# Kernel optimization log

Measured on AMD Instinct MI355X. Metric: run time of the kernel, lower is better.

Reference implementation:

```python
import jax, jax.numpy as jnp
import numpy as np

WS = 8          # window size
HEADS = 12      # attention heads
DIM = 768
HEAD_DIM = DIM // HEADS
EPS = 1e-5      # torch nn.LayerNorm default


def _layernorm(x, w, b):
    m = x.mean(-1, keepdims=True)
    v = ((x - m) ** 2).mean(-1, keepdims=True)
    return (x - m) / jnp.sqrt(v + EPS) * w + b


def setup_inputs() -> dict:
    key = jax.random.key(0)
    ks = jax.random.split(key, 8)
    s = 0.02  # weight init scale for numerical sanity
    dim, hd, ws = DIM, HEAD_DIM, WS
    return {
        "x": jax.random.normal(ks[0], (2, 16, 16, 16, dim), jnp.float32),
        "w_qkv": jax.random.normal(ks[1], (dim, 3 * dim), jnp.float32) * s,
        "b_qkv": jnp.zeros((3 * dim,), jnp.float32),
        "w_proj": jax.random.normal(ks[2], (dim, dim), jnp.float32) * s,
        "b_proj": jnp.zeros((dim,), jnp.float32),
        "rel_pos_d": jax.random.normal(ks[3], (2 * ws - 1, hd), jnp.float32) * s,
        "rel_pos_h": jax.random.normal(ks[4], (2 * ws - 1, hd), jnp.float32) * s,
        "rel_pos_w": jax.random.normal(ks[5], (2 * ws - 1, hd), jnp.float32) * s,
        "norm1_w": jnp.ones((dim,), jnp.float32),
        "norm1_b": jnp.zeros((dim,), jnp.float32),
        "norm2_w": jnp.ones((dim,), jnp.float32),
        "norm2_b": jnp.zeros((dim,), jnp.float32),
        "w1": jax.random.normal(ks[6], (dim, 4 * dim), jnp.float32) * s,
        "b1": jnp.zeros((4 * dim,), jnp.float32),
        "w2": jax.random.normal(ks[7], (4 * dim, dim), jnp.float32) * s,
        "b2": jnp.zeros((dim,), jnp.float32),
    }


def reference(x, w_qkv, b_qkv, w_proj, b_proj, rel_pos_d, rel_pos_h, rel_pos_w,
              norm1_w, norm1_b, norm2_w, norm2_b, w1, b1, w2, b2):
    B, D, H, W, C = x.shape
    ws, h = WS, HEADS
    hd = C // h
    scale = hd ** -0.5
    N = ws ** 3

    shortcut = x
    xn = _layernorm(x, norm1_w, norm1_b)

    # window partition (dims divide evenly -> no padding)
    xw = xn.reshape(B, D // ws, ws, H // ws, ws, W // ws, ws, C)
    xw = xw.transpose(0, 1, 3, 5, 2, 4, 6, 7).reshape(-1, N, C)  # [Bw, N, C]
    Bw = xw.shape[0]

    qkv = (xw @ w_qkv + b_qkv).reshape(Bw, N, 3, h, hd)
    qkv = qkv.transpose(2, 0, 3, 1, 4).reshape(3, Bw * h, N, hd)
    q, k, v = qkv[0], qkv[1], qkv[2]  # each [Bw*h, N, hd]

    attn = jnp.einsum('bqc,bkc->bqk', q * scale, k)  # [Bw*h, N, N]

    # decomposed relative position bias; q_size == k_size == ws, so no interp
    idx = jnp.arange(ws)[:, None] - jnp.arange(ws)[None, :] + (ws - 1)  # [ws, ws]
    Rd, Rh, Rw = rel_pos_d[idx], rel_pos_h[idx], rel_pos_w[idx]  # [ws, ws, hd]
    rq = q.reshape(Bw * h, ws, ws, ws, hd)
    rel_d = jnp.einsum('bdhwc,dkc->bdhwk', rq, Rd)
    rel_h = jnp.einsum('bdhwc,hkc->bdhwk', rq, Rh)
    rel_w = jnp.einsum('bdhwc,wkc->bdhwk', rq, Rw)
    attn = (attn.reshape(Bw * h, ws, ws, ws, ws, ws, ws)
            + rel_d[:, :, :, :, :, None, None]
            + rel_h[:, :, :, :, None, :, None]
            + rel_w[:, :, :, :, None, None, :]).reshape(Bw * h, N, N)

    attn = jax.nn.softmax(attn, axis=-1)
    out = (attn @ v).reshape(Bw, h, ws, ws, ws, hd)
    out = out.transpose(0, 2, 3, 4, 1, 5).reshape(Bw, N, C)
    out = out @ w_proj + b_proj

    # window unpartition
    out = out.reshape(B, D // ws, H // ws, W // ws, ws, ws, ws, C)
    out = out.transpose(0, 1, 4, 2, 5, 3, 6, 7).reshape(B, D, H, W, C)

    x = shortcut + out
    xn2 = _layernorm(x, norm2_w, norm2_b)
    # torch nn.GELU default is exact erf GELU
    x = x + (jax.nn.gelu(xn2 @ w1 + b1, approximate=False) @ w2 + b2)
    return x
```

## Files before the change

### kernel.cpp

```cpp
#include <hip/hip_runtime.h>
#include <hip/hip_bf16.h>
#include <math.h>

typedef short s16x8 __attribute__((ext_vector_type(8)));
typedef float f32x4 __attribute__((ext_vector_type(4)));
typedef int   s32x4 __attribute__((ext_vector_type(4)));

#define DIM 768
#define HEADS 12

static __device__ __forceinline__ short f2bf(float x) {
    union { float f; unsigned u; } v; v.f = x;
    unsigned r = (v.u + 0x7FFF + ((v.u >> 16) & 1)) >> 16;
    return (short)r;
}
static __device__ __forceinline__ float bf2f(short x) {
    union { unsigned u; float f; } v;
    v.u = ((unsigned)(unsigned short)x) << 16;
    return v.f;
}
static __device__ __forceinline__ unsigned cvt_pk_bf16(float lo, float hi) {
    unsigned r;
    asm("v_cvt_pk_bf16_f32 %0, %1, %2" : "=v"(r) : "v"(lo), "v"(hi));
    return r;
}

#define GLDS16(g, l) __builtin_amdgcn_global_load_lds( \
    (__attribute__((address_space(1))) void*)(g), \
    (__attribute__((address_space(3))) void*)(l), 16, 0, 0)

static __device__ __forceinline__ int nat_row(int t) {
    int w = t >> 9, n = t & 511;
    int b = w >> 3, dO = (w >> 2) & 1, hO = (w >> 1) & 1, wO = w & 1;
    int di = n >> 6, hi = (n >> 3) & 7, wi = n & 7;
    int Dd = dO * 8 + di, Hh = hO * 8 + hi, Ww = wO * 8 + wi;
    return ((b * 16 + Dd) * 16 + Hh) * 16 + Ww;
}

__global__ __launch_bounds__(256) void transpose_cvt(
    const float* __restrict__ in, short* __restrict__ out, int K, int N) {
    __shared__ float tile[32][33];
    int n0 = blockIdx.x * 32, k0 = blockIdx.y * 32;
    int tx = threadIdx.x & 31, ty = threadIdx.x >> 5;
#pragma unroll
    for (int j = 0; j < 4; j++) {
        int r = ty + j * 8;
        tile[r][tx] = in[(size_t)(k0 + r) * N + n0 + tx];
    }
    __syncthreads();
#pragma unroll
    for (int j = 0; j < 4; j++) {
        int r = ty + j * 8;
        out[(size_t)(n0 + r) * K + k0 + tx] = f2bf(tile[tx][r]);
    }
}

template<int PART>
__global__ __launch_bounds__(256) void ln_kernel(
    const float* __restrict__ x, const float* __restrict__ gw,
    const float* __restrict__ gb, short* __restrict__ out) {
    int t = blockIdx.x;
    int row = PART ? nat_row(t) : t;
    const float* xr = x + (size_t)row * DIM;
    float v0 = xr[threadIdx.x], v1 = xr[threadIdx.x + 256], v2 = xr[threadIdx.x + 512];
    float s1 = v0 + v1 + v2;
    float s2 = v0 * v0 + v1 * v1 + v2 * v2;
#pragma unroll
    for (int o = 32; o > 0; o >>= 1) { s1 += __shfl_down(s1, o); s2 += __shfl_down(s2, o); }
    __shared__ float ws1[4], ws2[4];
    int wid = threadIdx.x >> 6, lane = threadIdx.x & 63;
    if (lane == 0) { ws1[wid] = s1; ws2[wid] = s2; }
    __syncthreads();
    s1 = ws1[0] + ws1[1] + ws1[2] + ws1[3];
    s2 = ws2[0] + ws2[1] + ws2[2] + ws2[3];
    float mean = s1 * (1.f / DIM);
    float var = s2 * (1.f / DIM) - mean * mean;
    float inv = rsqrtf(var + 1e-5f);
    short* orow = out + (size_t)t * DIM;
    orow[threadIdx.x]       = f2bf((v0 - mean) * inv * gw[threadIdx.x]       + gb[threadIdx.x]);
    orow[threadIdx.x + 256] = f2bf((v1 - mean) * inv * gw[threadIdx.x + 256] + gb[threadIdx.x + 256]);
    orow[threadIdx.x + 512] = f2bf((v2 - mean) * inv * gw[threadIdx.x + 512] + gb[threadIdx.x + 512]);
}

enum { EPI_C = 0, EPI_PROJ = 1, EPI_GELU = 2, EPI_MLP2 = 3 };

template<int EPI, int K, int N, int BN>
__global__ __launch_bounds__(256) void gemm_kernel(
    const short* __restrict__ A, const short* __restrict__ BT,
    const float* __restrict__ bias,
    const float* __restrict__ x_in, float* __restrict__ out_f,
    short* __restrict__ out_b) {
    constexpr int GX = N / BN;
    constexpr int NW = BN / 32;
    constexpr int NT = K / 64;
    __shared__ short As[2][128 * 64];
    __shared__ short Bs[2][BN * 64];
    int flat = blockIdx.x;
    int cpx = gridDim.x >> 3;
    int swz = (flat & 7) * cpx + (flat >> 3);
    int tile_n = swz % GX, tile_m = swz / GX;
    int tid = threadIdx.x;
    int wid = tid >> 6, lane = tid & 63, lr = lane & 15, lg = lane >> 4;
    int wr = wid >> 1, wc = wid & 1;
    f32x4 acc[4][NW] = {};
    const short* Arow = A + (size_t)(tile_m * 128) * K;
    const short* Brow = BT + (size_t)(tile_n * BN) * K;
    int swzS = ((lane & 7) ^ ((tid >> 3) & 7)) * 8;
    const short* gA[4]; int ldsOA[4];
#pragma unroll
    for (int i = 0; i < 4; i++) {
        int row = (i * 256 + tid) >> 3;
        gA[i] = Arow + (size_t)row * K + swzS;
        ldsOA[i] = (i * 256 + wid * 64) * 8;
    }
    const short* gB[NW]; int ldsOB[NW];
#pragma unroll
    for (int i = 0; i < NW; i++) {
        int row = (i * 256 + tid) >> 3;
        gB[i] = Brow + (size_t)row * K + swzS;
        ldsOB[i] = (i * 256 + wid * 64) * 8;
    }
    auto stage = [&](int buf, int k0) {
#pragma unroll
        for (int i = 0; i < 4; i++) GLDS16(gA[i] + k0, &As[buf][ldsOA[i]]);
#pragma unroll
        for (int i = 0; i < NW; i++) GLDS16(gB[i] + k0, &Bs[buf][ldsOB[i]]);
    };
    stage(0, 0);
    __syncthreads();
#pragma unroll 1
    for (int t = 0; t < NT; t++) {
        int cur = t & 1;
        if (t + 1 < NT) stage(cur ^ 1, (t + 1) * 64);
#pragma unroll
        for (int h = 0; h < 2; h++) {
            s16x8 af[4], bfr[NW];
#pragma unroll
            for (int m = 0; m < 4; m++) {
                int row = wr * 64 + m * 16 + lr;
                af[m] = *(const s16x8*)&As[cur][row * 64 + (((h * 4 + lg) ^ (lr & 7)) << 3)];
            }
#pragma unroll
            for (int n = 0; n < NW; n++) {
                int row = wc * (BN / 2) + n * 16 + lr;
                bfr[n] = *(const s16x8*)&Bs[cur][row * 64 + (((h * 4 + lg) ^ (lr & 7)) << 3)];
            }
#pragma unroll
            for (int m = 0; m < 4; m++)
#pragma unroll
                for (int n = 0; n < NW; n++)
                    acc[m][n] = __builtin_amdgcn_mfma_f32_16x16x32_bf16(af[m], bfr[n], acc[m][n], 0, 0, 0);
        }
        __syncthreads();
    }
#pragma unroll
    for (int m = 0; m < 4; m++)
#pragma unroll
        for (int n = 0; n < NW; n++)
#pragma unroll
            for (int r = 0; r < 4; r++) {
                int row = tile_m * 128 + wr * 64 + m * 16 + lg * 4 + r;
                int col = tile_n * BN + wc * (BN / 2) + n * 16 + lr;
                float v = acc[m][n][r] + bias[col];
                if (EPI == EPI_C) {
                    out_b[(size_t)row * N + col] = f2bf(v);
                } else if (EPI == EPI_PROJ) {
                    int nr = nat_row(row);
                    out_f[(size_t)nr * DIM + col] = v + x_in[(size_t)nr * DIM + col];
                } else if (EPI == EPI_GELU) {
                    float u = v * (0.7978845608f + 0.0356774081f * v * v);
                    float e = __expf(2.f * u);
                    float g = v - v * __builtin_amdgcn_rcpf(1.f + e);
                    out_b[(size_t)row * (size_t)N + col] = f2bf(g);
                } else {
                    out_f[(size_t)row * DIM + col] += v;
                }
            }
}

__global__ __launch_bounds__(256) void repack_vt(
    const short* __restrict__ qkv, short* __restrict__ vt) {
    __shared__ short tile[64][72];
    int ntb = blockIdx.x, wh = blockIdx.y;
    int win = wh / HEADS, h = wh % HEADS;
    const short* vbase = qkv + (size_t)(win * 512 + ntb * 64) * 2304 + 1536 + h * 64;
    int tid = threadIdx.x;
#pragma unroll
    for (int p = 0; p < 2; p++) {
        int idx = tid + p * 256;
        int tok = idx >> 3, vc = idx & 7;
        s16x8 v = *(const s16x8*)&vbase[(size_t)tok * 2304 + vc * 8];
#pragma unroll
        for (int j = 0; j < 8; j++) tile[vc * 8 + j][tok] = v[j];
    }
    __syncthreads();
#pragma unroll
    for (int p = 0; p < 2; p++) {
        int idx = tid + p * 256;
        int d = idx >> 3, vc = idx & 7;
        s16x8 o = *(const s16x8*)&tile[d][vc * 8];
        *(s16x8*)&vt[((size_t)wh * 64 + d) * 512 + ntb * 64 + vc * 8] = o;
    }
}

__global__ __launch_bounds__(256) void attn_kernel(
    const short* __restrict__ qkv, const short* __restrict__ vt,
    const float* __restrict__ rpd, const float* __restrict__ rph,
    const float* __restrict__ rpw, short* __restrict__ out) {
    __shared__ float bdT[8][128], bhT[8][128], bwT[8][128];
    __shared__ short Rs[48 * 64];
    __shared__ short Ks[2][64 * 64];
    __shared__ short Vs[2][64 * 64];
    int qt2 = blockIdx.x;
    int wh = blockIdx.y;
    int win = wh / HEADS, h = wh % HEADS;
    int qbase = qt2 * 128;
    const short* qp = qkv + (size_t)(win * 512) * 2304 + h * 64;
    const short* kp = qp + 768;
    const short* vp = vt + (size_t)wh * 64 * 512;
    int tid = threadIdx.x, wid = tid >> 6, lane = tid & 63, lr = lane & 15, lg = lane >> 4;
    const float LOG2E = 1.4426950408889634f;

    s16x8 aq[2][2];
#pragma unroll
    for (int g = 0; g < 2; g++) {
        size_t qoff = (size_t)(qbase + g * 64 + wid * 16 + lr) * 2304;
        aq[g][0] = *(const s16x8*)&qp[qoff + lg * 8];
        aq[g][1] = *(const s16x8*)&qp[qoff + 32 + lg * 8];
    }

    for (int i = tid; i < 48 * 64; i += 256) {
        int row = i >> 6, c = i & 63;
        float v = 0.f;
        if (row < 9)                     v = rpd[(qt2 * 2 + row) * 64 + c];
        else if (row >= 16 && row < 31)  v = rph[(row - 16) * 64 + c];
        else if (row >= 32 && row < 47)  v = rpw[(row - 32) * 64 + c];
        Rs[row * 64 + ((((c >> 3) ^ (row & 7)) << 3) | (c & 7))] = f2bf(v * LOG2E);
    }
    __syncthreads();

    int row0 = wid * 8 + (lane >> 3);
    int swz = ((lane & 7) ^ (row0 & 7)) * 8;
    const short* kSrc0 = kp + (size_t)row0 * 2304 + swz;
    const short* kSrc1 = kp + (size_t)(row0 + 32) * 2304 + swz;
    const short* vSrc0 = vp + (size_t)row0 * 512 + swz;
    const short* vSrc1 = vp + (size_t)(row0 + 32) * 512 + swz;
    int ldsOff0 = wid * 512, ldsOff1 = 2048 + wid * 512;

    GLDS16(kSrc0, &Ks[0][ldsOff0]);
    GLDS16(kSrc1, &Ks[0][ldsOff1]);
    GLDS16(vSrc0, &Vs[0][ldsOff0]);
    GLDS16(vSrc1, &Vs[0][ldsOff1]);

    {
        f32x4 G[3][2];
#pragma unroll
        for (int t = 0; t < 3; t++) {
            int arow = t * 16 + lr;
            s16x8 a0 = *(const s16x8*)&Rs[arow * 64 + ((lg ^ (arow & 7)) << 3)];
            s16x8 a1 = *(const s16x8*)&Rs[arow * 64 + (((4 + lg) ^ (arow & 7)) << 3)];
#pragma unroll
            for (int g = 0; g < 2; g++) {
                f32x4 z = {};
                z = __builtin_amdgcn_mfma_f32_16x16x32_bf16(a0, aq[g][0], z, 0, 0, 0);
                z = __builtin_amdgcn_mfma_f32_16x16x32_bf16(a1, aq[g][1], z, 0, 0, 0);
                G[t][g] = z;
            }
        }
        int qcH = (wid * 2 + (lr >> 3)) & 7;
        int qcW = lr & 7;
#pragma unroll
        for (int g = 0; g < 2; g++) {
            int qr = g * 64 + wid * 16 + lr;
#pragma unroll
            for (int r = 0; r < 4; r++) {
                int j = lg * 4 + r;
                int kd = g + 7 - j;
                if (kd >= 0 && kd < 8) bdT[kd][qr] = G[0][g][r];
                int kh = qcH + 7 - j;
                if (kh >= 0 && kh < 8) bhT[kh][qr] = G[1][g][r];
                int kw = qcW + 7 - j;
                if (kw >= 0 && kw < 8) bwT[kw][qr] = G[2][g][r];
            }
        }
    }
    __syncthreads();

    float m_run[2] = {-1e30f, -1e30f}, l_run[2] = {0.f, 0.f};
    f32x4 accO[2][4] = {};
    int sel = lg >> 1;
    const float SC = 0.125f * LOG2E;

#pragma unroll 1
    for (int kt = 0; kt < 8; kt++) {
        int cur = kt & 1;
        if (kt < 7) {
            size_t kAdv = (size_t)(kt + 1) * 64 * 2304;
            int vAdv = (kt + 1) * 64;
            GLDS16(kSrc0 + kAdv, &Ks[cur ^ 1][ldsOff0]);
            GLDS16(kSrc1 + kAdv, &Ks[cur ^ 1][ldsOff1]);
            GLDS16(vSrc0 + vAdv, &Vs[cur ^ 1][ldsOff0]);
            GLDS16(vSrc1 + vAdv, &Vs[cur ^ 1][ldsOff1]);
        }
        f32x4 sa[2][4];
#pragma unroll
        for (int kn = 0; kn < 4; kn++) {
            int krow = kn * 16 + lr;
            const short* kb_ = &Ks[cur][krow * 64];
            s16x8 ak0 = *(const s16x8*)&kb_[((lg ^ (krow & 7)) << 3)];
            s16x8 ak1 = *(const s16x8*)&kb_[(((4 + lg) ^ (krow & 7)) << 3)];
#pragma unroll
            for (int g = 0; g < 2; g++) {
                f32x4 z = {};
                z = __builtin_amdgcn_mfma_f32_16x16x32_bf16(ak0, aq[g][0], z, 0, 0, 0);
                z = __builtin_amdgcn_mfma_f32_16x16x32_bf16(ak1, aq[g][1], z, 0, 0, 0);
                sa[g][kn] = z;
            }
        }
        s32x4 pb[2][2];
#pragma unroll
        for (int g = 0; g < 2; g++) {
            int qr = g * 64 + wid * 16 + lr;
            float bdv = bdT[kt][qr];
            float bb[4], bwv[4];
#pragma unroll
            for (int kn = 0; kn < 4; kn++) bb[kn] = bdv + bhT[2 * kn + sel][qr];
#pragma unroll
            for (int r = 0; r < 4; r++) bwv[r] = bwT[4 * (lg & 1) + r][qr];
            float sv[4][4], mx = -1e30f;
#pragma unroll
            for (int kn = 0; kn < 4; kn++)
#pragma unroll
                for (int r = 0; r < 4; r++) {
                    float vv = sa[g][kn][r] * SC + (bb[kn] + bwv[r]);
                    sv[kn][r] = vv;
                    mx = fmaxf(mx, vv);
                }
            mx = fmaxf(mx, __shfl_xor(mx, 16));
            mx = fmaxf(mx, __shfl_xor(mx, 32));
            float nm = fmaxf(m_run[g], mx);
            float corr = exp2f(m_run[g] - nm);
            m_run[g] = nm;
            float p[4][4], tsum = 0.f;
#pragma unroll
            for (int kn = 0; kn < 4; kn++)
#pragma unroll
                for (int r = 0; r < 4; r++) {
                    float pv = exp2f(sv[kn][r] - nm);
                    p[kn][r] = pv; tsum += pv;
                }
            tsum += __shfl_xor(tsum, 16);
            tsum += __shfl_xor(tsum, 32);
            l_run[g] = l_run[g] * corr + tsum;
#pragma unroll
            for (int n = 0; n < 4; n++)
#pragma unroll
                for (int r = 0; r < 4; r++) accO[g][n][r] *= corr;
            unsigned u[4][2];
#pragma unroll
            for (int kn = 0; kn < 4; kn++) {
                u[kn][0] = cvt_pk_bf16(p[kn][0], p[kn][1]);
                u[kn][1] = cvt_pk_bf16(p[kn][2], p[kn][3]);
            }
#pragma unroll
            for (int s2 = 0; s2 < 2; s2++)
#pragma unroll
                for (int tp = 0; tp < 2; tp++) {
                    int src = (2 * (lg & 1) + tp) * 16 + lr;
#pragma unroll
                    for (int j = 0; j < 2; j++) {
                        int a0 = __shfl((int)u[2 * s2][j], src);
                        int a1 = __shfl((int)u[2 * s2 + 1][j], src);
                        pb[g][s2][tp * 2 + j] = sel ? a1 : a0;
                    }
                }
        }
#pragma unroll
        for (int s2 = 0; s2 < 2; s2++) {
            s16x8 pb0 = *(s16x8*)&pb[0][s2];
            s16x8 pb1 = *(s16x8*)&pb[1][s2];
#pragma unroll
            for (int n = 0; n < 4; n++) {
                int vrow = n * 16 + lr;
                s16x8 av = *(const s16x8*)&Vs[cur][vrow * 64 + (((s2 * 4 + lg) ^ (vrow & 7)) << 3)];
                accO[0][n] = __builtin_amdgcn_mfma_f32_16x16x32_bf16(av, pb0, accO[0][n], 0, 0, 0);
                accO[1][n] = __builtin_amdgcn_mfma_f32_16x16x32_bf16(av, pb1, accO[1][n], 0, 0, 0);
            }
        }
        __syncthreads();
    }
#pragma unroll
    for (int g = 0; g < 2; g++) {
        float inv = __builtin_amdgcn_rcpf(l_run[g]);
        int tok = win * 512 + qbase + g * 64 + wid * 16 + lr;
        short* orow = out + (size_t)tok * DIM + h * 64;
#pragma unroll
        for (int n = 0; n < 4; n++)
#pragma unroll
            for (int j = 0; j < 2; j++) {
                unsigned uo = cvt_pk_bf16(accO[g][n][2 * j] * inv, accO[g][n][2 * j + 1] * inv);
                *(unsigned*)&orow[n * 16 + 4 * lg + 2 * j] = uo;
            }
    }
}

extern "C" void kernel_launch(void* const* d_in, const int* in_sizes, int n_in,
                              void* d_out, int out_size, void* d_ws, size_t ws_size,
                              hipStream_t stream) {
    const float* x      = (const float*)d_in[0];
    const float* w_qkv  = (const float*)d_in[1];
    const float* b_qkv  = (const float*)d_in[2];
    const float* w_proj = (const float*)d_in[3];
    const float* b_proj = (const float*)d_in[4];
    const float* rpd    = (const float*)d_in[5];
    const float* rph    = (const float*)d_in[6];
    const float* rpw    = (const float*)d_in[7];
    const float* n1w    = (const float*)d_in[8];
    const float* n1b    = (const float*)d_in[9];
    const float* n2w    = (const float*)d_in[10];
    const float* n2b    = (const float*)d_in[11];
    const float* w1     = (const float*)d_in[12];
    const float* b1     = (const float*)d_in[13];
    const float* w2     = (const float*)d_in[14];
    const float* b2     = (const float*)d_in[15];
    float* out = (float*)d_out;
    char* ws = (char*)d_ws;
    size_t off = 0;
    auto alloc = [&](size_t bytes) { void* p = ws + off; off += (bytes + 255) & ~255ULL; return p; };
    short* wqkvT  = (short*)alloc((size_t)2304 * 768 * 2);
    short* wprojT = (short*)alloc((size_t)768 * 768 * 2);
    short* w1T    = (short*)alloc((size_t)3072 * 768 * 2);
    short* w2T    = (short*)alloc((size_t)768 * 3072 * 2);
    short* xn1    = (short*)alloc((size_t)8192 * 768 * 2);
    short* qkvC   = (short*)alloc((size_t)8192 * 2304 * 2);
    short* vtb    = (short*)alloc((size_t)192 * 64 * 512 * 2);
    short* xn2    = (short*)alloc((size_t)8192 * 768 * 2);
    short* hid    = (short*)alloc((size_t)8192 * 3072 * 2);
    short* attnout = xn1;

    transpose_cvt<<<dim3(2304 / 32, 768 / 32), 256, 0, stream>>>(w_qkv, wqkvT, 768, 2304);
    transpose_cvt<<<dim3(768 / 32, 768 / 32), 256, 0, stream>>>(w_proj, wprojT, 768, 768);
    transpose_cvt<<<dim3(3072 / 32, 768 / 32), 256, 0, stream>>>(w1, w1T, 768, 3072);
    transpose_cvt<<<dim3(768 / 32, 3072 / 32), 256, 0, stream>>>(w2, w2T, 3072, 768);

    ln_kernel<1><<<8192, 256, 0, stream>>>(x, n1w, n1b, xn1);
    gemm_kernel<EPI_C, 768, 2304, 128><<<18 * 64, 256, 0, stream>>>(
        xn1, wqkvT, b_qkv, nullptr, nullptr, qkvC);
    repack_vt<<<dim3(8, 192), 256, 0, stream>>>(qkvC, vtb);
    attn_kernel<<<dim3(4, 192), 256, 0, stream>>>(qkvC, vtb, rpd, rph, rpw, attnout);
    gemm_kernel<EPI_PROJ, 768, 768, 64><<<12 * 64, 256, 0, stream>>>(
        attnout, wprojT, b_proj, x, out, nullptr);
    ln_kernel<0><<<8192, 256, 0, stream>>>(out, n2w, n2b, xn2);
    gemm_kernel<EPI_GELU, 768, 3072, 128><<<24 * 64, 256, 0, stream>>>(
        xn2, w1T, b1, nullptr, nullptr, hid);
    gemm_kernel<EPI_MLP2, 3072, 768, 64><<<12 * 64, 256, 0, stream>>>(
        hid, w2T, b2, nullptr, out, nullptr);
}
```

Before: 256.7 us.

## Triple-buffer GEMM K-loop with explicit vmcnt waits and XCD-aware tile mapping

Reworks the shared bf16 GEMM kernel into a three-stage LDS pipeline with 32-wide K steps. It waits on outstanding global-to-LDS loads with explicit s_waitcnt vmcnt and raw s_barrier instead of __syncthreads, so two tiles stay in flight while one is computed. It also replaces the block-index swizzle with a mapping that gives each XCD a contiguous rectangle of output tiles, aiming for better L2 reuse. This costs more barriers per K step, a changed LDS swizzle pattern, and a hand-tuned wait scheme that depends on the exact count of loads issued.

Measured after the change: 283.3 us. +10.4%, slower.

```diff
diff --git a/kernel.cpp b/kernel.cpp
--- a/kernel.cpp
+++ b/kernel.cpp
@@ -28,6 +28,15 @@
 #define GLDS16(g, l) __builtin_amdgcn_global_load_lds( \
     (__attribute__((address_space(1))) void*)(g), \
     (__attribute__((address_space(3))) void*)(l), 16, 0, 0)
+
+template<int Nw> static __device__ __forceinline__ void waitvm() {
+    if constexpr (Nw == 8)      asm volatile("s_waitcnt vmcnt(8)" ::: "memory");
+    else if constexpr (Nw == 6) asm volatile("s_waitcnt vmcnt(6)" ::: "memory");
+    else if constexpr (Nw == 4) asm volatile("s_waitcnt vmcnt(4)" ::: "memory");
+    else if constexpr (Nw == 3) asm volatile("s_waitcnt vmcnt(3)" ::: "memory");
+    else                        asm volatile("s_waitcnt vmcnt(0)" ::: "memory");
+    __builtin_amdgcn_sched_barrier(0);
+}
 
 static __device__ __forceinline__ int nat_row(int t) {
     int w = t >> 9, n = t & 511;
@@ -91,68 +100,86 @@
     const float* __restrict__ x_in, float* __restrict__ out_f,
     short* __restrict__ out_b) {
     constexpr int GX = N / BN;
+    constexpr int GM = 64;
     constexpr int NW = BN / 32;
-    constexpr int NT = K / 64;
-    __shared__ short As[2][128 * 64];
-    __shared__ short Bs[2][BN * 64];
+    constexpr int NT = K / 32;
+    constexpr int LA = 2, LB = BN / 64, L = LA + LB;
+    __shared__ short As[3][128 * 32];
+    __shared__ short Bs[3][BN * 32];
     int flat = blockIdx.x;
-    int cpx = gridDim.x >> 3;
-    int swz = (flat & 7) * cpx + (flat >> 3);
-    int tile_n = swz % GX, tile_m = swz / GX;
+    int xcd = flat & 7, idx = flat >> 3;
+    constexpr int TN = GX / 2, TM = GM / 4;
+    int tile_m = (xcd >> 1) * TM + idx / TN;
+    int tile_n = (xcd & 1) * TN + idx % TN;
     int tid = threadIdx.x;
     int wid = tid >> 6, lane = tid & 63, lr = lane & 15, lg = lane >> 4;
     int wr = wid >> 1, wc = wid & 1;
     f32x4 acc[4][NW] = {};
     const short* Arow = A + (size_t)(tile_m * 128) * K;
     const short* Brow = BT + (size_t)(tile_n * BN) * K;
-    int swzS = ((lane & 7) ^ ((tid >> 3) & 7)) * 8;
-    const short* gA[4]; int ldsOA[4];
-#pragma unroll
-    for (int i = 0; i < 4; i++) {
-        int row = (i * 256 + tid) >> 3;
-        gA[i] = Arow + (size_t)row * K + swzS;
-        ldsOA[i] = (i * 256 + wid * 64) * 8;
-    }
-    const short* gB[NW]; int ldsOB[NW];
-#pragma unroll
-    for (int i = 0; i < NW; i++) {
-        int row = (i * 256 + tid) >> 3;
-        gB[i] = Brow + (size_t)row * K + swzS;
-        ldsOB[i] = (i * 256 + wid * 64) * 8;
-    }
-    auto stage = [&](int buf, int k0) {
-#pragma unroll
-        for (int i = 0; i < 4; i++) GLDS16(gA[i] + k0, &As[buf][ldsOA[i]]);
-#pragma unroll
-        for (int i = 0; i < NW; i++) GLDS16(gB[i] + k0, &Bs[buf][ldsOB[i]]);
+    int srcq = ((tid & 3) ^ ((tid >> 3) & 3)) * 8;
+    const short* gA[LA]; const short* gB[LB];
+    int ldsA[LA], ldsB[LB];
+#pragma unroll
+    for (int i = 0; i < LA; i++) {
+        gA[i] = Arow + (size_t)(i * 64 + (tid >> 2)) * K + srcq;
+        ldsA[i] = (i * 256 + wid * 64) * 8;
+    }
+#pragma unroll
+    for (int i = 0; i < LB; i++) {
+        gB[i] = Brow + (size_t)(i * 64 + (tid >> 2)) * K + srcq;
+        ldsB[i] = (i * 256 + wid * 64) * 8;
+    }
+    auto stage = [&](int buf, int t) {
+        int k0 = t * 32;
+#pragma unroll
+        for (int i = 0; i < LA; i++) GLDS16(gA[i] + k0, &As[buf][ldsA[i]]);
+#pragma unroll
+        for (int i = 0; i < LB; i++) GLDS16(gB[i] + k0, &Bs[buf][ldsB[i]]);
     };
-    stage(0, 0);
-    __syncthreads();
+    auto compute = [&](int buf) {
+        s16x8 af[4], bfr[NW];
+#pragma unroll
+        for (int m = 0; m < 4; m++) {
+            int row = wr * 64 + m * 16 + lr;
+            af[m] = *(const s16x8*)&As[buf][row * 32 + ((lg ^ ((lr >> 1) & 3)) << 3)];
+        }
+#pragma unroll
+        for (int n = 0; n < NW; n++) {
+            int row = wc * (BN / 2) + n * 16 + lr;
+            bfr[n] = *(const s16x8*)&Bs[buf][row * 32 + ((lg ^ ((lr >> 1) & 3)) << 3)];
+        }
+#pragma unroll
+        for (int m = 0; m < 4; m++)
+#pragma unroll
+            for (int n = 0; n < NW; n++)
+                acc[m][n] = __builtin_amdgcn_mfma_f32_16x16x32_bf16(af[m], bfr[n], acc[m][n], 0, 0, 0);
+    };
+    stage(0, 0); stage(1, 1);
 #pragma unroll 1
-    for (int t = 0; t < NT; t++) {
-        int cur = t & 1;
-        if (t + 1 < NT) stage(cur ^ 1, (t + 1) * 64);
-#pragma unroll
-        for (int h = 0; h < 2; h++) {
-            s16x8 af[4], bfr[NW];
-#pragma unroll
-            for (int m = 0; m < 4; m++) {
-                int row = wr * 64 + m * 16 + lr;
-                af[m] = *(const s16x8*)&As[cur][row * 64 + (((h * 4 + lg) ^ (lr & 7)) << 3)];
-            }
-#pragma unroll
-            for (int n = 0; n < NW; n++) {
-                int row = wc * (BN / 2) + n * 16 + lr;
-                bfr[n] = *(const s16x8*)&Bs[cur][row * 64 + (((h * 4 + lg) ^ (lr & 7)) << 3)];
-            }
-#pragma unroll
-            for (int m = 0; m < 4; m++)
-#pragma unroll
-                for (int n = 0; n < NW; n++)
-                    acc[m][n] = __builtin_amdgcn_mfma_f32_16x16x32_bf16(af[m], bfr[n], acc[m][n], 0, 0, 0);
-        }
-        __syncthreads();
-    }
+    for (int tt = 0; tt < NT - 3; tt += 3) {
+        stage(2, tt + 2);
+        waitvm<2 * L>(); __builtin_amdgcn_s_barrier(); __builtin_amdgcn_sched_barrier(0);
+        compute(0);
+        __builtin_amdgcn_s_barrier();
+        stage(0, tt + 3);
+        waitvm<2 * L>(); __builtin_amdgcn_s_barrier(); __builtin_amdgcn_sched_barrier(0);
+        compute(1);
+        __builtin_amdgcn_s_barrier();
+        stage(1, tt + 4);
+        waitvm<2 * L>(); __builtin_amdgcn_s_barrier(); __builtin_amdgcn_sched_barrier(0);
+        compute(2);
+        __builtin_amdgcn_s_barrier();
+    }
+    stage(2, NT - 1);
+    waitvm<2 * L>(); __builtin_amdgcn_s_barrier(); __builtin_amdgcn_sched_barrier(0);
+    compute(0);
+    __builtin_amdgcn_s_barrier();
+    waitvm<L>(); __builtin_amdgcn_s_barrier(); __builtin_amdgcn_sched_barrier(0);
+    compute(1);
+    __builtin_amdgcn_s_barrier();
+    waitvm<0>(); __builtin_amdgcn_s_barrier(); __builtin_amdgcn_sched_barrier(0);
+    compute(2);
 #pragma unroll
     for (int m = 0; m < 4; m++)
 #pragma unroll
@@ -444,15 +471,15 @@
     transpose_cvt<<<dim3(768 / 32, 3072 / 32), 256, 0, stream>>>(w2, w2T, 3072, 768);
 
     ln_kernel<1><<<8192, 256, 0, stream>>>(x, n1w, n1b, xn1);
-    gemm_kernel<EPI_C, 768, 2304, 128><<<18 * 64, 256, 0, stream>>>(
+    gemm_kernel<EPI_C, 768, 2304, 128><<<64 * 18, 256, 0, stream>>>(
         xn1, wqkvT, b_qkv, nullptr, nullptr, qkvC);
     repack_vt<<<dim3(8, 192), 256, 0, stream>>>(qkvC, vtb);
     attn_kernel<<<dim3(4, 192), 256, 0, stream>>>(qkvC, vtb, rpd, rph, rpw, attnout);
-    gemm_kernel<EPI_PROJ, 768, 768, 64><<<12 * 64, 256, 0, stream>>>(
+    gemm_kernel<EPI_PROJ, 768, 768, 64><<<64 * 12, 256, 0, stream>>>(
         attnout, wprojT, b_proj, x, out, nullptr);
     ln_kernel<0><<<8192, 256, 0, stream>>>(out, n2w, n2b, xn2);
-    gemm_kernel<EPI_GELU, 768, 3072, 128><<<24 * 64, 256, 0, stream>>>(
+    gemm_kernel<EPI_GELU, 768, 3072, 128><<<64 * 24, 256, 0, stream>>>(
         xn2, w1T, b1, nullptr, nullptr, hid);
-    gemm_kernel<EPI_MLP2, 3072, 768, 64><<<12 * 64, 256, 0, stream>>>(
+    gemm_kernel<EPI_MLP2, 3072, 768, 64><<<64 * 12, 256, 0, stream>>>(
         hid, w2T, b2, nullptr, out, nullptr);
 }
```

## Add 256x128 tile GEMM with K=32 stages for QKV and MLP1

Applied to the files above, without the earlier changes.

Adds a new gemm_big kernel that uses a 256x128 output tile with 32-wide K stages, double-buffered LDS, and an XOR swizzle. The QKV and first MLP GEMMs switch to it, raising arithmetic intensity per block and halving the grid size. The existing gemm_kernel's source swizzle is also changed to depend only on the lane. The larger tile raises register pressure (32 accumulators per lane), and the shallower K stage means more sync points.

Result: faster. 249.8 us (-2.7%).

```diff
diff --git a/kernel.cpp b/kernel.cpp
--- a/kernel.cpp
+++ b/kernel.cpp
@@ -105,7 +105,7 @@
     f32x4 acc[4][NW] = {};
     const short* Arow = A + (size_t)(tile_m * 128) * K;
     const short* Brow = BT + (size_t)(tile_n * BN) * K;
-    int swzS = ((lane & 7) ^ ((tid >> 3) & 7)) * 8;
+    int swzS = ((lane & 7) ^ (lane >> 3)) * 8;
     const short* gA[4]; int ldsOA[4];
 #pragma unroll
     for (int i = 0; i < 4; i++) {
@@ -174,6 +174,88 @@
                     out_b[(size_t)row * (size_t)N + col] = f2bf(g);
                 } else {
                     out_f[(size_t)row * DIM + col] += v;
+                }
+            }
+}
+
+template<int EPI, int K, int N>
+__global__ __launch_bounds__(256, 2) void gemm_big(
+    const short* __restrict__ A, const short* __restrict__ BT,
+    const float* __restrict__ bias, short* __restrict__ out_b) {
+    constexpr int GX = N / 128;
+    constexpr int NT = K / 32;
+    __shared__ short As[2][256 * 32];
+    __shared__ short Bs[2][128 * 32];
+    int flat = blockIdx.x;
+    int cpx = gridDim.x >> 3;
+    int swz = (flat & 7) * cpx + (flat >> 3);
+    int tile_n = swz % GX, tile_m = swz / GX;
+    int tid = threadIdx.x;
+    int wid = tid >> 6, lane = tid & 63, lr = lane & 15, lg = lane >> 4;
+    int wr = wid >> 1, wc = wid & 1;
+    f32x4 acc[8][4] = {};
+    const short* Arow = A + (size_t)(tile_m * 256) * K;
+    const short* Brow = BT + (size_t)(tile_n * 128) * K;
+    int srcq = ((tid & 3) ^ ((tid >> 3) & 3)) * 8;
+    const short* gA[4]; const short* gB[2];
+    int ldsA[4], ldsB[2];
+#pragma unroll
+    for (int i = 0; i < 4; i++) {
+        gA[i] = Arow + (size_t)(i * 64 + (tid >> 2)) * K + srcq;
+        ldsA[i] = (i * 256 + wid * 64) * 8;
+    }
+#pragma unroll
+    for (int i = 0; i < 2; i++) {
+        gB[i] = Brow + (size_t)(i * 64 + (tid >> 2)) * K + srcq;
+        ldsB[i] = (i * 256 + wid * 64) * 8;
+    }
+    auto stage = [&](int buf, int t) {
+        int k0 = t * 32;
+#pragma unroll
+        for (int i = 0; i < 4; i++) GLDS16(gA[i] + k0, &As[buf][ldsA[i]]);
+#pragma unroll
+        for (int i = 0; i < 2; i++) GLDS16(gB[i] + k0, &Bs[buf][ldsB[i]]);
+    };
+    stage(0, 0);
+    __syncthreads();
+#pragma unroll 1
+    for (int t = 0; t < NT; t++) {
+        int cur = t & 1;
+        if (t + 1 < NT) stage(cur ^ 1, t + 1);
+        s16x8 af[8], bfr[4];
+#pragma unroll
+        for (int m = 0; m < 8; m++) {
+            int row = wr * 128 + m * 16 + lr;
+            af[m] = *(const s16x8*)&As[cur][row * 32 + ((lg ^ ((lr >> 1) & 3)) << 3)];
+        }
+#pragma unroll
+        for (int n = 0; n < 4; n++) {
+            int row = wc * 64 + n * 16 + lr;
+            bfr[n] = *(const s16x8*)&Bs[cur][row * 32 + ((lg ^ ((lr >> 1) & 3)) << 3)];
+        }
+#pragma unroll
+        for (int m = 0; m < 8; m++)
+#pragma unroll
+            for (int n = 0; n < 4; n++)
+                acc[m][n] = __builtin_amdgcn_mfma_f32_16x16x32_bf16(af[m], bfr[n], acc[m][n], 0, 0, 0);
+        __syncthreads();
+    }
+#pragma unroll
+    for (int m = 0; m < 8; m++)
+#pragma unroll
+        for (int n = 0; n < 4; n++)
+#pragma unroll
+            for (int r = 0; r < 4; r++) {
+                int row = tile_m * 256 + wr * 128 + m * 16 + lg * 4 + r;
+                int col = tile_n * 128 + wc * 64 + n * 16 + lr;
+                float v = acc[m][n][r] + bias[col];
+                if (EPI == EPI_C) {
+                    out_b[(size_t)row * N + col] = f2bf(v);
+                } else {
+                    float u = v * (0.7978845608f + 0.0356774081f * v * v);
+                    float e = __expf(2.f * u);
+                    float g = v - v * __builtin_amdgcn_rcpf(1.f + e);
+                    out_b[(size_t)row * (size_t)N + col] = f2bf(g);
                 }
             }
 }
@@ -444,15 +526,13 @@
     transpose_cvt<<<dim3(768 / 32, 3072 / 32), 256, 0, stream>>>(w2, w2T, 3072, 768);
 
     ln_kernel<1><<<8192, 256, 0, stream>>>(x, n1w, n1b, xn1);
-    gemm_kernel<EPI_C, 768, 2304, 128><<<18 * 64, 256, 0, stream>>>(
-        xn1, wqkvT, b_qkv, nullptr, nullptr, qkvC);
+    gemm_big<EPI_C, 768, 2304><<<576, 256, 0, stream>>>(xn1, wqkvT, b_qkv, qkvC);
     repack_vt<<<dim3(8, 192), 256, 0, stream>>>(qkvC, vtb);
     attn_kernel<<<dim3(4, 192), 256, 0, stream>>>(qkvC, vtb, rpd, rph, rpw, attnout);
-    gemm_kernel<EPI_PROJ, 768, 768, 64><<<12 * 64, 256, 0, stream>>>(
+    gemm_kernel<EPI_PROJ, 768, 768, 64><<<64 * 12, 256, 0, stream>>>(
         attnout, wprojT, b_proj, x, out, nullptr);
     ln_kernel<0><<<8192, 256, 0, stream>>>(out, n2w, n2b, xn2);
-    gemm_kernel<EPI_GELU, 768, 3072, 128><<<24 * 64, 256, 0, stream>>>(
-        xn2, w1T, b1, nullptr, nullptr, hid);
-    gemm_kernel<EPI_MLP2, 3072, 768, 64><<<12 * 64, 256, 0, stream>>>(
+    gemm_big<EPI_GELU, 768, 3072><<<768, 256, 0, stream>>>(xn2, w1T, b1, hid);
+    gemm_kernel<EPI_MLP2, 3072, 768, 64><<<64 * 12, 256, 0, stream>>>(
         hid, w2T, b2, nullptr, out, nullptr);
 }
```

## Add 256x256 eight-wave pipelined GEMM for QKV and MLP1 projections

Applied to the files above, without the earlier changes.

Adds a new GEMM kernel with 512 threads, 256x256 output tiles and K split into two 32-wide halves. Each half is double-buffered in LDS and loaded through global_load_lds, interleaved with MFMA phases under explicit barriers, wave priority and vmcnt gating. It replaces the 128-tile GEMM for the QKV and first MLP layers, aiming for more data reuse per block and better overlap of loads with compute. The global-source swizzle in the old GEMM is also changed to depend only on the lane. The larger tile launches fewer blocks (288 and 384) on a 256-CU part, which risks wave-quantization tail effects and uses large register and LDS budgets.

New measurement: 274.7 us. +7.0%, slower.

```diff
diff --git a/kernel.cpp b/kernel.cpp
--- a/kernel.cpp
+++ b/kernel.cpp
@@ -28,6 +28,8 @@
 #define GLDS16(g, l) __builtin_amdgcn_global_load_lds( \
     (__attribute__((address_space(1))) void*)(g), \
     (__attribute__((address_space(3))) void*)(l), 16, 0, 0)
+
+#define ASM_BARRIER asm volatile("s_barrier" ::: "memory")
 
 static __device__ __forceinline__ int nat_row(int t) {
     int w = t >> 9, n = t & 511;
@@ -105,7 +107,7 @@
     f32x4 acc[4][NW] = {};
     const short* Arow = A + (size_t)(tile_m * 128) * K;
     const short* Brow = BT + (size_t)(tile_n * BN) * K;
-    int swzS = ((lane & 7) ^ ((tid >> 3) & 7)) * 8;
+    int swzS = ((lane & 7) ^ (lane >> 3)) * 8;
     const short* gA[4]; int ldsOA[4];
 #pragma unroll
     for (int i = 0; i < 4; i++) {
@@ -176,6 +178,102 @@
                     out_f[(size_t)row * DIM + col] += v;
                 }
             }
+}
+
+template<int EPI, int K, int N>
+__global__ __launch_bounds__(512, 1) void gemm_p8(
+    const short* __restrict__ A, const short* __restrict__ BT,
+    const float* __restrict__ bias, short* __restrict__ out_b) {
+    constexpr int NT = K / 64;
+    constexpr int GX = N / 256;
+    __shared__ short Al[2][2][256 * 32];
+    __shared__ short Bl[2][2][256 * 32];
+    int flat = blockIdx.x;
+    int cpx = gridDim.x >> 3;
+    int swz = (flat & 7) * cpx + (flat >> 3);
+    int tile_n = swz % GX, tile_m = swz / GX;
+    int tid = threadIdx.x, wid = tid >> 6, lane = tid & 63, lr = lane & 15, lg = lane >> 4;
+    int wm = wid >> 2, wn = wid & 3;
+    f32x4 acc[8][4] = {};
+    const short* Arow = A + (size_t)(tile_m * 256) * K;
+    const short* Brow = BT + (size_t)(tile_n * 256) * K;
+    int srcq = ((tid & 3) ^ ((tid >> 3) & 3)) * 8;
+    const short* aS0 = Arow + (size_t)(tid >> 2) * K + srcq;
+    const short* aS1 = Arow + (size_t)(128 + (tid >> 2)) * K + srcq;
+    const short* bS0 = Brow + (size_t)(tid >> 2) * K + srcq;
+    const short* bS1 = Brow + (size_t)(128 + (tid >> 2)) * K + srcq;
+    int wbase = wid * 512;
+    auto stA = [&](int buf, int kh, int t) {
+        int ko = t * 64 + kh * 32;
+        GLDS16(aS0 + ko, &Al[buf][kh][wbase]);
+        GLDS16(aS1 + ko, &Al[buf][kh][4096 + wbase]);
+    };
+    auto stB = [&](int buf, int kh, int t) {
+        int ko = t * 64 + kh * 32;
+        GLDS16(bS0 + ko, &Bl[buf][kh][wbase]);
+        GLDS16(bS1 + ko, &Bl[buf][kh][4096 + wbase]);
+    };
+    stB(0, 0, 0); stA(0, 0, 0); stB(0, 1, 0); stA(0, 1, 0);
+    stB(1, 0, 1); stA(1, 0, 1); stB(1, 1, 1);
+    asm volatile("s_waitcnt vmcnt(0)" ::: "memory");
+    ASM_BARRIER;
+    int aswz = (lr >> 1) & 3;
+    int arow0 = (wm * 128 + lr) * 32;
+    int brow0 = (wn * 64 + lr) * 32;
+    s16x8 bfr[4];
+#define P8_RDB(KH) { \
+    _Pragma("unroll") \
+    for (int n = 0; n < 4; n++) \
+        bfr[n] = *(const s16x8*)&Bl[buf][KH][brow0 + n * 512 + ((lg ^ aswz) << 3)]; }
+#define P8_PHASE(KH, B, STAGE, GATE) { \
+    if (B == 0) P8_RDB(KH); \
+    s16x8 af[4]; \
+    _Pragma("unroll") \
+    for (int m = 0; m < 4; m++) \
+        af[m] = *(const s16x8*)&Al[buf][KH][arow0 + (B * 64 + m * 16) * 32 + ((lg ^ aswz) << 3)]; \
+    STAGE; \
+    ASM_BARRIER; \
+    __builtin_amdgcn_s_setprio(1); \
+    _Pragma("unroll") \
+    for (int m = 0; m < 4; m++) \
+        _Pragma("unroll") \
+        for (int n = 0; n < 4; n++) \
+            acc[B * 4 + m][n] = __builtin_amdgcn_mfma_f32_16x16x32_bf16(af[m], bfr[n], acc[B * 4 + m][n], 0, 0, 0); \
+    __builtin_amdgcn_s_setprio(0); \
+    if (GATE) { \
+        if (late) { asm volatile("s_waitcnt vmcnt(0)" ::: "memory"); } \
+        else      { asm volatile("s_waitcnt vmcnt(10)" ::: "memory"); } \
+    } \
+    ASM_BARRIER; }
+#pragma unroll 1
+    for (int t = 0; t < NT; t++) {
+        int buf = t & 1, ot = buf ^ 1;
+        bool late = (t >= NT - 3);
+        P8_PHASE(0, 0, { if (t + 1 < NT) stA(ot, 1, t + 1); }, 0)
+        P8_PHASE(0, 1, { if (t + 2 < NT) stB(buf, 0, t + 2); }, 1)
+        P8_PHASE(1, 0, { if (t + 2 < NT) stA(buf, 0, t + 2); }, 0)
+        P8_PHASE(1, 1, { if (t + 2 < NT) stB(buf, 1, t + 2); }, 1)
+    }
+#pragma unroll
+    for (int M = 0; M < 8; M++)
+#pragma unroll
+        for (int n = 0; n < 4; n++)
+#pragma unroll
+            for (int r = 0; r < 4; r++) {
+                int row = tile_m * 256 + wm * 128 + M * 16 + lg * 4 + r;
+                int col = tile_n * 256 + wn * 64 + n * 16 + lr;
+                float v = acc[M][n][r] + bias[col];
+                if (EPI == EPI_C) {
+                    out_b[(size_t)row * N + col] = f2bf(v);
+                } else {
+                    float u = v * (0.7978845608f + 0.0356774081f * v * v);
+                    float e = __expf(2.f * u);
+                    float g = v - v * __builtin_amdgcn_rcpf(1.f + e);
+                    out_b[(size_t)row * (size_t)N + col] = f2bf(g);
+                }
+            }
+#undef P8_RDB
+#undef P8_PHASE
 }
 
 __global__ __launch_bounds__(256) void repack_vt(
@@ -444,15 +542,13 @@
     transpose_cvt<<<dim3(768 / 32, 3072 / 32), 256, 0, stream>>>(w2, w2T, 3072, 768);
 
     ln_kernel<1><<<8192, 256, 0, stream>>>(x, n1w, n1b, xn1);
-    gemm_kernel<EPI_C, 768, 2304, 128><<<18 * 64, 256, 0, stream>>>(
-        xn1, wqkvT, b_qkv, nullptr, nullptr, qkvC);
+    gemm_p8<EPI_C, 768, 2304><<<288, 512, 0, stream>>>(xn1, wqkvT, b_qkv, qkvC);
     repack_vt<<<dim3(8, 192), 256, 0, stream>>>(qkvC, vtb);
     attn_kernel<<<dim3(4, 192), 256, 0, stream>>>(qkvC, vtb, rpd, rph, rpw, attnout);
-    gemm_kernel<EPI_PROJ, 768, 768, 64><<<12 * 64, 256, 0, stream>>>(
+    gemm_kernel<EPI_PROJ, 768, 768, 64><<<64 * 12, 256, 0, stream>>>(
         attnout, wprojT, b_proj, x, out, nullptr);
     ln_kernel<0><<<8192, 256, 0, stream>>>(out, n2w, n2b, xn2);
-    gemm_kernel<EPI_GELU, 768, 3072, 128><<<24 * 64, 256, 0, stream>>>(
-        xn2, w1T, b1, nullptr, nullptr, hid);
-    gemm_kernel<EPI_MLP2, 3072, 768, 64><<<12 * 64, 256, 0, stream>>>(
+    gemm_p8<EPI_GELU, 768, 3072><<<384, 512, 0, stream>>>(xn2, w1T, b1, hid);
+    gemm_kernel<EPI_MLP2, 3072, 768, 64><<<64 * 12, 256, 0, stream>>>(
         hid, w2T, b2, nullptr, out, nullptr);
 }
```
